# Kernel optimization log

Measured on AMD Instinct MI355X. Metric: run time of the kernel, lower is better.

The kernel has to match this reference:

```python
import jax, jax.numpy as jnp
import numpy as np

N = 50000
F_IN = 256
D_HID = 64
H = 8
C = 10
E_RAND = 800000
ALPHA = 0.2  # leaky_relu negative slope


def setup_inputs() -> dict:
    key = jax.random.key(0)
    k = jax.random.split(key, 7)
    x = jax.random.normal(k[0], (N, F_IN), dtype=jnp.float32)
    # edge list = self-loops (ensure nonzero softmax denominator) + random edges
    self_idx = jnp.arange(N, dtype=jnp.int32)
    edge_src = jnp.concatenate([self_idx, jax.random.randint(k[1], (E_RAND,), 0, N, dtype=jnp.int32)])
    edge_dst = jnp.concatenate([self_idx, jax.random.randint(k[2], (E_RAND,), 0, N, dtype=jnp.int32)])
    W_heads = jax.random.normal(k[3], (H, F_IN, D_HID), dtype=jnp.float32) * 0.05
    a_heads = jax.random.normal(k[4], (H, 2 * D_HID), dtype=jnp.float32) * 0.05
    W_out = jax.random.normal(k[5], (H * D_HID, C), dtype=jnp.float32) * 0.05
    a_out = jax.random.normal(k[6], (2 * C,), dtype=jnp.float32) * 0.05
    return {"x": x, "edge_src": edge_src, "edge_dst": edge_dst,
            "W_heads": W_heads, "a_heads": a_heads, "W_out": W_out, "a_out": a_out}


def sp_gat_layer(x, W, a, src, dst, concat):
    """pyGAT SpGraphAttentionLayer (eval mode, dropout off)."""
    n = x.shape[0]
    d = W.shape[1]
    h = x @ W                                             # [N, d]
    score = h[src] @ a[:d] + h[dst] @ a[d:]               # [E] per-edge attention logit
    e = jnp.exp(-jax.nn.leaky_relu(score, ALPHA))         # unnormalized attention
    rowsum = jax.ops.segment_sum(e, src, num_segments=n)  # [N] softmax denominator
    agg = jax.ops.segment_sum(e[:, None] * h[dst], src, num_segments=n)  # [N, d]
    out = agg / rowsum[:, None]
    return jax.nn.elu(out) if concat else out


def reference(x, edge_src, edge_dst, W_heads, a_heads, W_out, a_out):
    # multi-head sparse attention, heads concatenated along feature dim
    heads = jax.vmap(lambda W, a: sp_gat_layer(x, W, a, edge_src, edge_dst, True))(W_heads, a_heads)  # [H, N, d]
    xcat = jnp.transpose(heads, (1, 0, 2)).reshape(x.shape[0], -1)  # [N, H*d]
    out = jax.nn.elu(sp_gat_layer(xcat, W_out, a_out, edge_src, edge_dst, False))  # [N, C]
    return jax.nn.log_softmax(out, axis=1)
```

## Files before the change

### kernel.cpp

```cpp
#include <hip/hip_runtime.h>
#include <hip/hip_bf16.h>

#define F_IN    256
#define D_HID   64
#define H_HEADS 8
#define NC      10
#define ALPHA   0.2f
#define FLAG_THRESH 64
#define SCAN_T  1024

typedef __attribute__((ext_vector_type(8))) short short8;
typedef __attribute__((ext_vector_type(4))) float f32x4;

__device__ __forceinline__ float bfu2f(unsigned short u) {
    union { float f; unsigned int i; } c; c.i = ((unsigned int)u) << 16; return c.f;
}
__device__ __forceinline__ unsigned short f2bfu(float f) {
    union { float f; unsigned int i; } c; c.f = f;
    unsigned int x = c.i;
    x += 0x7fffu + ((x >> 16) & 1u);
    return (unsigned short)(x >> 16);
}

__global__ void detect_kernel(const unsigned int* __restrict__ x, int* __restrict__ flag) {
    int t = threadIdx.x;
    int cnt = 0;
    for (int i = t; i < 4096; i += 256) {
        unsigned int w = x[i];
        unsigned int e = (w >> 7) & 0xffu;
        if (e >= 140u) cnt++;
    }
    atomicAdd(flag, cnt);
}

__global__ __launch_bounds__(256) void convert_kernel(
    const void* __restrict__ src, float* __restrict__ dst, long n,
    const int* __restrict__ flagp)
{
    long i = (long)blockIdx.x * 256 + threadIdx.x;
    if (i >= n) return;
    bool isf32 = (*flagp > FLAG_THRESH);
    dst[i] = isf32 ? ((const float*)src)[i]
                   : bfu2f(((const unsigned short*)src)[i]);
}

__global__ __launch_bounds__(256) void convert_x_kernel(
    const void* __restrict__ src, unsigned short* __restrict__ dst, long n8,
    const int* __restrict__ flagp)
{
    long i = (long)blockIdx.x * 256 + threadIdx.x;
    if (i >= n8) return;
    bool isf32 = (*flagp > FLAG_THRESH);
    unsigned short o[8];
    if (isf32) {
        const float* s = (const float*)src + i * 8;
        #pragma unroll
        for (int j = 0; j < 8; ++j) o[j] = f2bfu(s[j]);
    } else {
        *(uint4*)o = ((const uint4*)src)[i];
    }
    *(uint4*)(dst + i * 8) = *(uint4*)o;
}

__global__ __launch_bounds__(256) void convert_whT_kernel(
    const void* __restrict__ src, unsigned short* __restrict__ dst,
    const int* __restrict__ flagp)
{
    int i = blockIdx.x * 256 + threadIdx.x;
    if (i >= H_HEADS * F_IN * D_HID) return;
    int d = i & 63, k = (i >> 6) & 255, h = i >> 14;
    bool isf32 = (*flagp > FLAG_THRESH);
    float v = isf32 ? ((const float*)src)[i] : bfu2f(((const unsigned short*)src)[i]);
    dst[(h * 64 + d) * 256 + k] = f2bfu(v);
}

__global__ __launch_bounds__(256) void hist_kernel(
    const int* __restrict__ src, int* __restrict__ counts, int E)
{
    int e = blockIdx.x * 256 + threadIdx.x;
    if (e < E) atomicAdd(&counts[src[e]], 1);
}

__global__ __launch_bounds__(SCAN_T) void scan_kernel(
    const int* __restrict__ counts, int* __restrict__ row_start, int N, int E)
{
    __shared__ int sums[SCAN_T];
    int t = threadIdx.x;
    int chunk = (N + SCAN_T - 1) / SCAN_T;
    int b = t * chunk, e = min(b + chunk, N);
    int s = 0;
    for (int i = b; i < e; ++i) s += counts[i];
    sums[t] = s;
    __syncthreads();
    for (int off = 1; off < SCAN_T; off <<= 1) {
        int u = (t >= off) ? sums[t - off] : 0;
        __syncthreads();
        sums[t] += u;
        __syncthreads();
    }
    int running = sums[t] - s;
    for (int i = b; i < e; ++i) { row_start[i] = running; running += counts[i]; }
    if (t == SCAN_T - 1) row_start[N] = E;
}

__global__ __launch_bounds__(256) void scatter_ev_kernel(
    const int* __restrict__ src, const int* __restrict__ dst,
    const int* __restrict__ row_start, int* __restrict__ cursor,
    const float* __restrict__ s1s, const float* __restrict__ s1d,
    int* __restrict__ csr_dst, float* __restrict__ ev_csr, int E)
{
    int e = blockIdx.x * 256 + threadIdx.x;
    if (e >= E) return;
    int s = src[e], d = dst[e];
    int pos = atomicAdd(&cursor[s], 1);
    int i = row_start[s] + pos;
    csr_dst[i] = d;
    float4 ss0 = *(const float4*)(s1s + s * 8);
    float4 ss1 = *(const float4*)(s1s + s * 8 + 4);
    float4 sd0 = *(const float4*)(s1d + d * 8);
    float4 sd1 = *(const float4*)(s1d + d * 8 + 4);
    float sc[8] = { ss0.x + sd0.x, ss0.y + sd0.y, ss0.z + sd0.z, ss0.w + sd0.w,
                    ss1.x + sd1.x, ss1.y + sd1.y, ss1.z + sd1.z, ss1.w + sd1.w };
    float ev[8];
    #pragma unroll
    for (int h = 0; h < 8; ++h) {
        float lr = sc[h] > 0.f ? sc[h] : ALPHA * sc[h];
        ev[h] = __expf(-lr);
    }
    *(float4*)(ev_csr + (long)i * 8)     = make_float4(ev[0], ev[1], ev[2], ev[3]);
    *(float4*)(ev_csr + (long)i * 8 + 4) = make_float4(ev[4], ev[5], ev[6], ev[7]);
}

__global__ __launch_bounds__(256) void gemm1_kernel(
    const unsigned short* __restrict__ x_bf,
    const unsigned short* __restrict__ wh_t,
    const float* __restrict__ ah,
    unsigned short* __restrict__ h_bf,
    float* __restrict__ s1s, float* __restrict__ s1d, int N)
{
    __shared__ unsigned short Os[64][72];

    const int t = threadIdx.x;
    const int w = t >> 6, lane = t & 63;
    const int q = lane >> 4, m = lane & 15;
    const int n0 = blockIdx.x * 64;
    const int h = blockIdx.y;

    int r = n0 + 16 * w + m;
    const unsigned short* xr = x_bf + (long)(r < N ? r : N - 1) * 256;
    short8 afrag[8];
    #pragma unroll
    for (int ks = 0; ks < 8; ++ks)
        afrag[ks] = *(const short8*)(xr + ks * 32 + q * 8);

    f32x4 acc[4] = {};
    const unsigned short* Bh = wh_t + (long)h * 64 * 256;
    #pragma unroll
    for (int ks = 0; ks < 8; ++ks) {
        #pragma unroll
        for (int c = 0; c < 4; ++c) {
            short8 b = *(const short8*)(Bh + (c * 16 + m) * 256 + ks * 32 + q * 8);
            acc[c] = __builtin_amdgcn_mfma_f32_16x16x32_bf16(afrag[ks], b, acc[c], 0, 0, 0);
        }
    }

    const float* a1 = ah + h * 128;
    float a1m = a1[m], a1m16 = a1[16 + m], a1m32 = a1[32 + m], a1m48 = a1[48 + m];
    float a2m = a1[64 + m], a2m16 = a1[80 + m], a2m32 = a1[96 + m], a2m48 = a1[112 + m];
    #pragma unroll
    for (int reg = 0; reg < 4; ++reg) {
        float p1 = acc[0][reg] * a1m + acc[1][reg] * a1m16 + acc[2][reg] * a1m32 + acc[3][reg] * a1m48;
        float p2 = acc[0][reg] * a2m + acc[1][reg] * a2m16 + acc[2][reg] * a2m32 + acc[3][reg] * a2m48;
        #pragma unroll
        for (int off = 1; off < 16; off <<= 1) {
            p1 += __shfl_xor(p1, off);
            p2 += __shfl_xor(p2, off);
        }
        int row = n0 + 16 * w + q * 4 + reg;
        if (m == 0 && row < N) {
            s1s[row * 8 + h] = p1;
            s1d[row * 8 + h] = p2;
        }
    }

    #pragma unroll
    for (int c = 0; c < 4; ++c)
        #pragma unroll
        for (int reg = 0; reg < 4; ++reg)
            Os[16 * w + q * 4 + reg][c * 16 + m] = f2bfu(acc[c][reg]);
    #pragma unroll
    for (int j = 0; j < 2; ++j) {
        int cc = j * 64 + lane;
        int row = cc >> 3, c8 = cc & 7;
        if (n0 + 16 * w + row < N)
            *(uint4*)(h_bf + (long)(n0 + 16 * w + row) * 512 + h * 64 + c8 * 8) =
                *(const uint4*)&Os[16 * w + row][c8 * 8];
    }
}

__global__ __launch_bounds__(256) void edge_agg1_kernel(
    const int* __restrict__ row_start, const int* __restrict__ csr_dst,
    const float* __restrict__ ev_csr,
    const uint4* __restrict__ h_q,
    uint4* __restrict__ xcat_q,
    int N)
{
    int lane = threadIdx.x & 63;
    int n = blockIdx.x * 4 + (threadIdx.x >> 6);
    if (n >= N) return;
    int h = lane >> 3;
    int beg = row_start[n], end = row_start[n + 1];

    float acc[8] = {0.f, 0.f, 0.f, 0.f, 0.f, 0.f, 0.f, 0.f};
    float rs = 0.f;
    int dnext = csr_dst[beg];
    for (int i = beg; i < end; ++i) {
        int d = dnext;
        if (i + 1 < end) dnext = csr_dst[i + 1];
        float ev = ev_csr[(long)i * 8 + h];
        uint4 wv = h_q[(long)d * 64 + lane];
        rs += ev;
        acc[0] += ev * bfu2f((unsigned short)(wv.x & 0xffffu));
        acc[1] += ev * bfu2f((unsigned short)(wv.x >> 16));
        acc[2] += ev * bfu2f((unsigned short)(wv.y & 0xffffu));
        acc[3] += ev * bfu2f((unsigned short)(wv.y >> 16));
        acc[4] += ev * bfu2f((unsigned short)(wv.z & 0xffffu));
        acc[5] += ev * bfu2f((unsigned short)(wv.z >> 16));
        acc[6] += ev * bfu2f((unsigned short)(wv.w & 0xffffu));
        acc[7] += ev * bfu2f((unsigned short)(wv.w >> 16));
    }
    float inv = 1.f / rs;
    unsigned short o[8];
    #pragma unroll
    for (int j = 0; j < 8; ++j) {
        float v = acc[j] * inv;
        v = v > 0.f ? v : __expf(v) - 1.f;
        o[j] = f2bfu(v);
    }
    xcat_q[(long)n * 64 + lane] = *(const uint4*)o;
}

__global__ __launch_bounds__(256) void gemm2_kernel(
    const unsigned short* __restrict__ xcat_bf,
    const float* __restrict__ Wo,
    const float* __restrict__ ao,
    float* __restrict__ h2p,
    float* __restrict__ s2s, float* __restrict__ s2d, int N)
{
    int n = blockIdx.x * 256 + threadIdx.x;
    if (n >= N) return;
    float acc[NC];
    #pragma unroll
    for (int c = 0; c < NC; ++c) acc[c] = 0.f;
    const uint4* xp = (const uint4*)(xcat_bf + (long)n * 512);
    for (int k8 = 0; k8 < 64; ++k8) {
        uint4 w = xp[k8];
        float f[8];
        f[0] = bfu2f((unsigned short)(w.x & 0xffffu)); f[1] = bfu2f((unsigned short)(w.x >> 16));
        f[2] = bfu2f((unsigned short)(w.y & 0xffffu)); f[3] = bfu2f((unsigned short)(w.y >> 16));
        f[4] = bfu2f((unsigned short)(w.z & 0xffffu)); f[5] = bfu2f((unsigned short)(w.z >> 16));
        f[6] = bfu2f((unsigned short)(w.w & 0xffffu)); f[7] = bfu2f((unsigned short)(w.w >> 16));
        #pragma unroll
        for (int u = 0; u < 8; ++u) {
            const float* wr = Wo + (k8 * 8 + u) * NC;
            #pragma unroll
            for (int c = 0; c < NC; ++c) acc[c] += f[u] * wr[c];
        }
    }
    float s1 = 0.f, s2 = 0.f;
    *(float4*)(h2p + (long)n * 16)      = make_float4(acc[0], acc[1], acc[2], acc[3]);
    *(float4*)(h2p + (long)n * 16 + 4)  = make_float4(acc[4], acc[5], acc[6], acc[7]);
    *(float4*)(h2p + (long)n * 16 + 8)  = make_float4(acc[8], acc[9], 0.f, 0.f);
    *(float4*)(h2p + (long)n * 16 + 12) = make_float4(0.f, 0.f, 0.f, 0.f);
    #pragma unroll
    for (int c = 0; c < NC; ++c) {
        s1 += acc[c] * ao[c];
        s2 += acc[c] * ao[NC + c];
    }
    s2s[n] = s1;
    s2d[n] = s2;
}

__global__ __launch_bounds__(256) void edge_agg2_kernel(
    const int* __restrict__ row_start, const int* __restrict__ csr_dst,
    const float* __restrict__ h2p,
    const float* __restrict__ s_src2, const float* __restrict__ s_dst2,
    void* __restrict__ out, const int* __restrict__ flagp, int N)
{
    int lane = threadIdx.x & 63;
    int n = blockIdx.x * 4 + (threadIdx.x >> 6);
    if (n >= N) return;
    int c = lane & 15, j = lane >> 4;
    int beg = row_start[n], end = row_start[n + 1];
    float ss = s_src2[n];
    float rs = 0.f, acc = 0.f;
    for (int i0 = beg; i0 < end; i0 += 4) {
        int i = i0 + j;
        if (i < end) {
            int d = csr_dst[i];
            float sc = ss + s_dst2[d];
            float lr = sc > 0.f ? sc : ALPHA * sc;
            float ev = __expf(-lr);
            rs += ev;
            acc += ev * h2p[(long)d * 16 + c];
        }
    }
    rs  += __shfl_xor(rs, 16, 64);  rs  += __shfl_xor(rs, 32, 64);
    acc += __shfl_xor(acc, 16, 64); acc += __shfl_xor(acc, 32, 64);
    float v = acc / rs;
    v = v > 0.f ? v : __expf(v) - 1.f;
    float vm = (c < NC) ? v : -1e30f;
    #pragma unroll
    for (int off = 1; off < 16; off <<= 1) vm = fmaxf(vm, __shfl_xor(vm, off, 64));
    float ex = (c < NC) ? __expf(v - vm) : 0.f;
    #pragma unroll
    for (int off = 1; off < 16; off <<= 1) ex += __shfl_xor(ex, off, 64);
    float lse = vm + logf(ex);
    if (c < NC && j == 0) {
        bool isf32 = (*flagp > FLAG_THRESH);
        if (isf32) ((float*)out)[(long)n * NC + c] = v - lse;
        else       ((unsigned short*)out)[(long)n * NC + c] = f2bfu(v - lse);
    }
}

extern "C" void kernel_launch(void* const* d_in, const int* in_sizes, int n_in,
                              void* d_out, int out_size, void* d_ws, size_t ws_size,
                              hipStream_t stream)
{
    const void* x_raw  = d_in[0];
    const int*  esrc   = (const int*)d_in[1];
    const int*  edst   = (const int*)d_in[2];
    const void* Wh_raw = d_in[3];
    const void* ah_raw = d_in[4];
    const void* Wo_raw = d_in[5];
    const void* ao_raw = d_in[6];

    const int N = in_sizes[0] / F_IN;
    const int E = in_sizes[1];

    char* ws = (char*)d_ws;
    size_t off = 0;
    auto alloc = [&](size_t bytes) -> void* {
        void* p = ws + off;
        off = (off + bytes + 255) & ~(size_t)255;
        return p;
    };
    int*            flag      = (int*)           alloc(4);
    unsigned short* x_bf      = (unsigned short*)alloc((size_t)N * F_IN * 2);
    unsigned short* wh_t      = (unsigned short*)alloc((size_t)H_HEADS * D_HID * F_IN * 2);
    float*          ah32      = (float*)         alloc((size_t)H_HEADS * 2 * D_HID * 4);
    float*          Wo32      = (float*)         alloc((size_t)512 * NC * 4);
    float*          ao32      = (float*)         alloc((size_t)2 * NC * 4);
    unsigned short* h_bf      = (unsigned short*)alloc((size_t)N * 512 * 2);
    unsigned short* xcat_bf   = (unsigned short*)alloc((size_t)N * 512 * 2);
    float*          s1s       = (float*)         alloc((size_t)N * 8 * 4);
    float*          s1d       = (float*)         alloc((size_t)N * 8 * 4);
    float*          h2p       = (float*)         alloc((size_t)N * 16 * 4);
    float*          s2s       = (float*)         alloc((size_t)N * 4);
    float*          s2d       = (float*)         alloc((size_t)N * 4);
    int*            counts    = (int*)           alloc((size_t)N * 4);
    int*            cursor    = (int*)           alloc((size_t)N * 4);
    int*            row_start = (int*)           alloc((size_t)(N + 1) * 4);
    int*            csr_dst   = (int*)           alloc((size_t)E * 4);
    float*          ev_csr    = (float*)         alloc((size_t)E * 8 * 4);
    (void)ws_size;

    hipMemsetAsync(flag, 0, 4, stream);
    hipMemsetAsync(counts, 0, (size_t)N * 4, stream);
    hipMemsetAsync(cursor, 0, (size_t)N * 4, stream);

    detect_kernel<<<1, 256, 0, stream>>>((const unsigned int*)x_raw, flag);
    long n8 = (long)N * F_IN / 8;
    convert_x_kernel<<<(unsigned)((n8 + 255) / 256), 256, 0, stream>>>(x_raw, x_bf, n8, flag);
    convert_whT_kernel<<<(H_HEADS * F_IN * D_HID + 255) / 256, 256, 0, stream>>>(Wh_raw, wh_t, flag);
    convert_kernel<<<(H_HEADS * 2 * D_HID + 255) / 256, 256, 0, stream>>>(ah_raw, ah32, H_HEADS * 2 * D_HID, flag);
    convert_kernel<<<(512 * NC + 255) / 256, 256, 0, stream>>>(Wo_raw, Wo32, 512 * NC, flag);
    convert_kernel<<<1, 256, 0, stream>>>(ao_raw, ao32, 2 * NC, flag);

    hist_kernel<<<(E + 255) / 256, 256, 0, stream>>>(esrc, counts, E);
    scan_kernel<<<1, SCAN_T, 0, stream>>>(counts, row_start, N, E);

    dim3 g1((N + 63) / 64, H_HEADS);
    gemm1_kernel<<<g1, 256, 0, stream>>>(x_bf, wh_t, ah32, h_bf, s1s, s1d, N);
    scatter_ev_kernel<<<(E + 255) / 256, 256, 0, stream>>>(esrc, edst, row_start, cursor,
                                                           s1s, s1d, csr_dst, ev_csr, E);
    edge_agg1_kernel<<<(N + 3) / 4, 256, 0, stream>>>(row_start, csr_dst, ev_csr,
                                                      (const uint4*)h_bf, (uint4*)xcat_bf, N);

    gemm2_kernel<<<(N + 255) / 256, 256, 0, stream>>>(xcat_bf, Wo32, ao32, h2p, s2s, s2d, N);
    edge_agg2_kernel<<<(N + 3) / 4, 256, 0, stream>>>(row_start, csr_dst, h2p, s2s, s2d, d_out, flag, N);
}
```

Measured before the change: 598.5 us.

## Fuse prep conversions and histogram into one launch, merge memsets, two heads per GEMM block

Merges the x, W_heads, a_heads, W_out and a_out conversion kernels and the edge histogram into a single block-partitioned prep kernel. Places flag, counts and cursor next to each other so one memset clears all three. Changes gemm1 so each block computes two heads, reusing the A fragments loaded once and halving the number of x row reads. This cuts launch overhead and redundant x traffic, at the cost of more registers per gemm1 block and fewer blocks in its grid.

```diff
diff --git a/kernel.cpp b/kernel.cpp
--- a/kernel.cpp
+++ b/kernel.cpp
@@ -33,52 +33,51 @@
     atomicAdd(flag, cnt);
 }
 
-__global__ __launch_bounds__(256) void convert_kernel(
-    const void* __restrict__ src, float* __restrict__ dst, long n,
-    const int* __restrict__ flagp)
-{
-    long i = (long)blockIdx.x * 256 + threadIdx.x;
-    if (i >= n) return;
+__global__ __launch_bounds__(256) void prep_kernel(
+    const void* __restrict__ x_raw,  unsigned short* __restrict__ x_bf,
+    const void* __restrict__ Wh_raw, unsigned short* __restrict__ wh_t,
+    const void* __restrict__ ah_raw, float* __restrict__ ah32,
+    const void* __restrict__ Wo_raw, float* __restrict__ Wo32,
+    const void* __restrict__ ao_raw, float* __restrict__ ao32,
+    const int* __restrict__ esrc, int* __restrict__ counts,
+    const int* __restrict__ flagp, int N, int E,
+    int bx, int bw, int ba, int bo)
+{
+    int b = blockIdx.x;
     bool isf32 = (*flagp > FLAG_THRESH);
-    dst[i] = isf32 ? ((const float*)src)[i]
-                   : bfu2f(((const unsigned short*)src)[i]);
-}
-
-__global__ __launch_bounds__(256) void convert_x_kernel(
-    const void* __restrict__ src, unsigned short* __restrict__ dst, long n8,
-    const int* __restrict__ flagp)
-{
-    long i = (long)blockIdx.x * 256 + threadIdx.x;
-    if (i >= n8) return;
-    bool isf32 = (*flagp > FLAG_THRESH);
-    unsigned short o[8];
-    if (isf32) {
-        const float* s = (const float*)src + i * 8;
-        #pragma unroll
-        for (int j = 0; j < 8; ++j) o[j] = f2bfu(s[j]);
+    if (b < bx) {
+        long i = (long)b * 256 + threadIdx.x;
+        long n8 = (long)N * F_IN / 8;
+        if (i < n8) {
+            unsigned short o[8];
+            if (isf32) {
+                const float* s = (const float*)x_raw + i * 8;
+                #pragma unroll
+                for (int j = 0; j < 8; ++j) o[j] = f2bfu(s[j]);
+            } else {
+                *(uint4*)o = ((const uint4*)x_raw)[i];
+            }
+            *(uint4*)(x_bf + i * 8) = *(uint4*)o;
+        }
+    } else if (b < bw) {
+        int i = (b - bx) * 256 + threadIdx.x;
+        int d = i & 63, k = (i >> 6) & 255, h = i >> 14;
+        float v = isf32 ? ((const float*)Wh_raw)[i] : bfu2f(((const unsigned short*)Wh_raw)[i]);
+        wh_t[(h * 64 + d) * 256 + k] = f2bfu(v);
+    } else if (b < ba) {
+        int i = (b - bw) * 256 + threadIdx.x;
+        ah32[i] = isf32 ? ((const float*)ah_raw)[i] : bfu2f(((const unsigned short*)ah_raw)[i]);
+    } else if (b < bo) {
+        int i = (b - ba) * 256 + threadIdx.x;
+        Wo32[i] = isf32 ? ((const float*)Wo_raw)[i] : bfu2f(((const unsigned short*)Wo_raw)[i]);
+    } else if (b == bo) {
+        int i = threadIdx.x;
+        if (i < 2 * NC)
+            ao32[i] = isf32 ? ((const float*)ao_raw)[i] : bfu2f(((const unsigned short*)ao_raw)[i]);
     } else {
-        *(uint4*)o = ((const uint4*)src)[i];
-    }
-    *(uint4*)(dst + i * 8) = *(uint4*)o;
-}
-
-__global__ __launch_bounds__(256) void convert_whT_kernel(
-    const void* __restrict__ src, unsigned short* __restrict__ dst,
-    const int* __restrict__ flagp)
-{
-    int i = blockIdx.x * 256 + threadIdx.x;
-    if (i >= H_HEADS * F_IN * D_HID) return;
-    int d = i & 63, k = (i >> 6) & 255, h = i >> 14;
-    bool isf32 = (*flagp > FLAG_THRESH);
-    float v = isf32 ? ((const float*)src)[i] : bfu2f(((const unsigned short*)src)[i]);
-    dst[(h * 64 + d) * 256 + k] = f2bfu(v);
-}
-
-__global__ __launch_bounds__(256) void hist_kernel(
-    const int* __restrict__ src, int* __restrict__ counts, int E)
-{
-    int e = blockIdx.x * 256 + threadIdx.x;
-    if (e < E) atomicAdd(&counts[src[e]], 1);
+        int e = (b - bo - 1) * 256 + threadIdx.x;
+        if (e < E) atomicAdd(&counts[esrc[e]], 1);
+    }
 }
 
 __global__ __launch_bounds__(SCAN_T) void scan_kernel(
@@ -144,7 +143,7 @@
     const int w = t >> 6, lane = t & 63;
     const int q = lane >> 4, m = lane & 15;
     const int n0 = blockIdx.x * 64;
-    const int h = blockIdx.y;
+    const int h0 = blockIdx.y * 2;
 
     int r = n0 + 16 * w + m;
     const unsigned short* xr = x_bf + (long)(r < N ? r : N - 1) * 256;
@@ -153,48 +152,52 @@
     for (int ks = 0; ks < 8; ++ks)
         afrag[ks] = *(const short8*)(xr + ks * 32 + q * 8);
 
-    f32x4 acc[4] = {};
-    const unsigned short* Bh = wh_t + (long)h * 64 * 256;
-    #pragma unroll
-    for (int ks = 0; ks < 8; ++ks) {
-        #pragma unroll
-        for (int c = 0; c < 4; ++c) {
-            short8 b = *(const short8*)(Bh + (c * 16 + m) * 256 + ks * 32 + q * 8);
-            acc[c] = __builtin_amdgcn_mfma_f32_16x16x32_bf16(afrag[ks], b, acc[c], 0, 0, 0);
-        }
-    }
-
-    const float* a1 = ah + h * 128;
-    float a1m = a1[m], a1m16 = a1[16 + m], a1m32 = a1[32 + m], a1m48 = a1[48 + m];
-    float a2m = a1[64 + m], a2m16 = a1[80 + m], a2m32 = a1[96 + m], a2m48 = a1[112 + m];
-    #pragma unroll
-    for (int reg = 0; reg < 4; ++reg) {
-        float p1 = acc[0][reg] * a1m + acc[1][reg] * a1m16 + acc[2][reg] * a1m32 + acc[3][reg] * a1m48;
-        float p2 = acc[0][reg] * a2m + acc[1][reg] * a2m16 + acc[2][reg] * a2m32 + acc[3][reg] * a2m48;
-        #pragma unroll
-        for (int off = 1; off < 16; off <<= 1) {
-            p1 += __shfl_xor(p1, off);
-            p2 += __shfl_xor(p2, off);
-        }
-        int row = n0 + 16 * w + q * 4 + reg;
-        if (m == 0 && row < N) {
-            s1s[row * 8 + h] = p1;
-            s1d[row * 8 + h] = p2;
-        }
-    }
-
-    #pragma unroll
-    for (int c = 0; c < 4; ++c)
-        #pragma unroll
-        for (int reg = 0; reg < 4; ++reg)
-            Os[16 * w + q * 4 + reg][c * 16 + m] = f2bfu(acc[c][reg]);
-    #pragma unroll
-    for (int j = 0; j < 2; ++j) {
-        int cc = j * 64 + lane;
-        int row = cc >> 3, c8 = cc & 7;
-        if (n0 + 16 * w + row < N)
-            *(uint4*)(h_bf + (long)(n0 + 16 * w + row) * 512 + h * 64 + c8 * 8) =
-                *(const uint4*)&Os[16 * w + row][c8 * 8];
+    #pragma unroll
+    for (int hi = 0; hi < 2; ++hi) {
+        const int h = h0 + hi;
+        f32x4 acc[4] = {};
+        const unsigned short* Bh = wh_t + (long)h * 64 * 256;
+        #pragma unroll
+        for (int ks = 0; ks < 8; ++ks) {
+            #pragma unroll
+            for (int c = 0; c < 4; ++c) {
+                short8 b = *(const short8*)(Bh + (c * 16 + m) * 256 + ks * 32 + q * 8);
+                acc[c] = __builtin_amdgcn_mfma_f32_16x16x32_bf16(afrag[ks], b, acc[c], 0, 0, 0);
+            }
+        }
+
+        const float* a1 = ah + h * 128;
+        float a1m = a1[m], a1m16 = a1[16 + m], a1m32 = a1[32 + m], a1m48 = a1[48 + m];
+        float a2m = a1[64 + m], a2m16 = a1[80 + m], a2m32 = a1[96 + m], a2m48 = a1[112 + m];
+        #pragma unroll
+        for (int reg = 0; reg < 4; ++reg) {
+            float p1 = acc[0][reg] * a1m + acc[1][reg] * a1m16 + acc[2][reg] * a1m32 + acc[3][reg] * a1m48;
+            float p2 = acc[0][reg] * a2m + acc[1][reg] * a2m16 + acc[2][reg] * a2m32 + acc[3][reg] * a2m48;
+            #pragma unroll
+            for (int off = 1; off < 16; off <<= 1) {
+                p1 += __shfl_xor(p1, off);
+                p2 += __shfl_xor(p2, off);
+            }
+            int row = n0 + 16 * w + q * 4 + reg;
+            if (m == 0 && row < N) {
+                s1s[row * 8 + h] = p1;
+                s1d[row * 8 + h] = p2;
+            }
+        }
+
+        #pragma unroll
+        for (int c = 0; c < 4; ++c)
+            #pragma unroll
+            for (int reg = 0; reg < 4; ++reg)
+                Os[16 * w + q * 4 + reg][c * 16 + m] = f2bfu(acc[c][reg]);
+        #pragma unroll
+        for (int j = 0; j < 2; ++j) {
+            int cc = j * 64 + lane;
+            int row = cc >> 3, c8 = cc & 7;
+            if (n0 + 16 * w + row < N)
+                *(uint4*)(h_bf + (long)(n0 + 16 * w + row) * 512 + h * 64 + c8 * 8) =
+                    *(const uint4*)&Os[16 * w + row][c8 * 8];
+        }
     }
 }
 
@@ -346,6 +349,10 @@
         return p;
     };
     int*            flag      = (int*)           alloc(4);
+    int*            counts    = (int*)           alloc((size_t)N * 4);
+    int*            cursor    = (int*)           alloc((size_t)N * 4);
+    size_t clear_span = (size_t)((char*)cursor + (size_t)N * 4 - (char*)flag);
+
     unsigned short* x_bf      = (unsigned short*)alloc((size_t)N * F_IN * 2);
     unsigned short* wh_t      = (unsigned short*)alloc((size_t)H_HEADS * D_HID * F_IN * 2);
     float*          ah32      = (float*)         alloc((size_t)H_HEADS * 2 * D_HID * 4);
@@ -358,29 +365,25 @@
     float*          h2p       = (float*)         alloc((size_t)N * 16 * 4);
     float*          s2s       = (float*)         alloc((size_t)N * 4);
     float*          s2d       = (float*)         alloc((size_t)N * 4);
-    int*            counts    = (int*)           alloc((size_t)N * 4);
-    int*            cursor    = (int*)           alloc((size_t)N * 4);
     int*            row_start = (int*)           alloc((size_t)(N + 1) * 4);
     int*            csr_dst   = (int*)           alloc((size_t)E * 4);
     float*          ev_csr    = (float*)         alloc((size_t)E * 8 * 4);
     (void)ws_size;
 
-    hipMemsetAsync(flag, 0, 4, stream);
-    hipMemsetAsync(counts, 0, (size_t)N * 4, stream);
-    hipMemsetAsync(cursor, 0, (size_t)N * 4, stream);
+    hipMemsetAsync(flag, 0, clear_span, stream);
 
     detect_kernel<<<1, 256, 0, stream>>>((const unsigned int*)x_raw, flag);
-    long n8 = (long)N * F_IN / 8;
-    convert_x_kernel<<<(unsigned)((n8 + 255) / 256), 256, 0, stream>>>(x_raw, x_bf, n8, flag);
-    convert_whT_kernel<<<(H_HEADS * F_IN * D_HID + 255) / 256, 256, 0, stream>>>(Wh_raw, wh_t, flag);
-    convert_kernel<<<(H_HEADS * 2 * D_HID + 255) / 256, 256, 0, stream>>>(ah_raw, ah32, H_HEADS * 2 * D_HID, flag);
-    convert_kernel<<<(512 * NC + 255) / 256, 256, 0, stream>>>(Wo_raw, Wo32, 512 * NC, flag);
-    convert_kernel<<<1, 256, 0, stream>>>(ao_raw, ao32, 2 * NC, flag);
-
-    hist_kernel<<<(E + 255) / 256, 256, 0, stream>>>(esrc, counts, E);
+    int bx = (int)(((long)N * F_IN / 8 + 255) / 256);
+    int bw = bx + (H_HEADS * F_IN * D_HID) / 256;
+    int ba = bw + (H_HEADS * 2 * D_HID) / 256;
+    int bo = ba + (512 * NC) / 256;
+    int nb = bo + 1 + (E + 255) / 256;
+    prep_kernel<<<nb, 256, 0, stream>>>(x_raw, x_bf, Wh_raw, wh_t, ah_raw, ah32,
+                                        Wo_raw, Wo32, ao_raw, ao32,
+                                        esrc, counts, flag, N, E, bx, bw, ba, bo);
     scan_kernel<<<1, SCAN_T, 0, stream>>>(counts, row_start, N, E);
 
-    dim3 g1((N + 63) / 64, H_HEADS);
+    dim3 g1((N + 63) / 64, H_HEADS / 2);
     gemm1_kernel<<<g1, 256, 0, stream>>>(x_bf, wh_t, ah32, h_bf, s1s, s1d, N);
     scatter_ev_kernel<<<(E + 255) / 256, 256, 0, stream>>>(esrc, edst, row_start, cursor,
                                                            s1s, s1d, csr_dst, ev_csr, E);
```

After: 585.1 us. -2.2%, faster.
